# Kernel optimization log

Measured on AMD Instinct MI355X. Metric: run time of the kernel, lower is better.

## Reference

```python
import jax, jax.numpy as jnp
import numpy as np

EPS = 1e-12  # matches torch F.normalize default eps
TARGET_N = 6.0  # target_compression_N


def _l2_normalize(v):
    n = jnp.linalg.norm(v, axis=-1, keepdims=True)
    return v / jnp.maximum(n, EPS)


def setup_inputs() -> dict:
    key = jax.random.key(0)
    k1, k2, k3 = jax.random.split(key, 3)
    B, L, D = 4, 8192, 1024
    x = jax.random.normal(k1, (B, L, D), dtype=jnp.float32)
    # nn.Linear weights (out, in), applied as x @ W.T
    Wq = jax.random.normal(k2, (D, D), dtype=jnp.float32) * (1.0 / np.sqrt(D))
    Wk = jax.random.normal(k3, (D, D), dtype=jnp.float32) * (1.0 / np.sqrt(D))
    return {"x": x, "Wq": Wq, "Wk": Wk}


def reference(x, Wq, Wk):
    B, L, D = x.shape
    q = jnp.einsum('bld,ed->ble', x, Wq)
    k = jnp.einsum('bld,ed->ble', x, Wk)
    q_norm = _l2_normalize(q)
    k_norm = _l2_normalize(k)
    k_prev = jnp.roll(k_norm, shift=1, axis=1)
    cos_sim = jnp.sum(q_norm * k_prev, axis=-1)          # (B, L)
    p = 0.5 * (1.0 - cos_sim)
    p = p.at[:, 0].set(1.0)
    b = (p >= 0.5).astype(x.dtype)
    b = b.at[:, 0].set(1.0)

    F_val = jnp.mean(b)
    G_val = jnp.mean(p)
    N = TARGET_N
    ratio_loss = N / (N - 1.0) * ((N - 1.0) * F_val * G_val + (1.0 - F_val) * (1.0 - G_val))

    # Stream compaction via cumsum-based scatter.  Lc_max is data dependent in
    # the torch code; for jit-compatibility we pad the compressed axis to L.
    mask = b > 0.5                                        # (B, L) bool
    dest = jnp.cumsum(b.astype(jnp.int32), axis=1) - 1   # destination slot per boundary
    dest = jnp.clip(dest, 0, L - 1)
    bidx = jnp.broadcast_to(jnp.arange(B, dtype=jnp.int32)[:, None], (B, L))
    # Non-boundary positions contribute exact zeros (x * mask), so colliding
    # destinations from clipped/non-boundary entries are harmless under add.
    x_down = jnp.zeros((B, L, D), dtype=x.dtype).at[bidx, dest].add(x * mask[..., None])
    P_down = jnp.zeros((B, L), dtype=p.dtype).at[bidx, dest].add(p * mask)
    lengths = jnp.sum(b, axis=1).astype(jnp.int32)        # (B,)

    return x_down, P_down, b, p, lengths, ratio_loss
```

## Files before the change

### kernel.cpp

```cpp
#include <hip/hip_runtime.h>
#include <stdint.h>
#include <stddef.h>

typedef __attribute__((ext_vector_type(8)))  _Float16 f16x8;
typedef __attribute__((ext_vector_type(16))) float    f32x16;
typedef __attribute__((ext_vector_type(4)))  float    f32x4;
typedef __attribute__((ext_vector_type(4)))  unsigned int u32x4;

#define B_ 4
#define L_ 8192
#define D_ 1024
#define BL 32768
#define XR 32768
#define XCV_BYTES (256u * XR * 16u)
#define WCV_BYTES (256u * 1024u * 16u)

__device__ __forceinline__ void gload16(const void* g, void* l){
  __builtin_amdgcn_global_load_lds((const __attribute__((address_space(1))) void*)g,
                                   (__attribute__((address_space(3))) void*)l, 16, 0, 0);
}

__device__ __forceinline__ f32x16 MF(f16x8 a, f16x8 b, f32x16 c){
  return __builtin_amdgcn_mfma_f32_32x32x16_f16(a, b, c, 0, 0, 0);
}

__global__ void k0_cvt(const float* __restrict__ x, const float* __restrict__ Wq,
                       const float* __restrict__ Wk, unsigned char* __restrict__ xcv)
{
  __shared__ unsigned short hi[64][128];
  __shared__ unsigned short lo[64][128];
  const int bx = blockIdx.x, kt = blockIdx.y, tid = threadIdx.x;
  const float* src; unsigned char* dst; int rs, rt;
  if (bx < 512){ src = x;  dst = xcv;                         rs = XR;   rt = bx; }
  else if (bx < 528){ src = Wq; dst = xcv + XCV_BYTES;        rs = 1024; rt = bx - 512; }
  else { src = Wk; dst = xcv + XCV_BYTES + WCV_BYTES;         rs = 1024; rt = bx - 528; }

  #pragma unroll
  for (int it = 0; it < 8; ++it){
    int idx = it*256 + tid;
    int r = idx >> 5, q4 = idx & 31;
    f32x4 v = *(const f32x4*)(src + (size_t)(rt*64 + r)*1024 + kt*128 + q4*4);
    int swb = ((q4 >> 1) ^ (r & 15))*8 + (q4 & 1)*4;
    #pragma unroll
    for (int j = 0; j < 4; ++j){
      float f = v[j];
      _Float16 h = (_Float16)f;
      _Float16 l = (_Float16)(f - (float)h);
      hi[r][swb + j] = __builtin_bit_cast(unsigned short, h);
      lo[r][swb + j] = __builtin_bit_cast(unsigned short, l);
    }
  }
  __syncthreads();
  #pragma unroll
  for (int it = 0; it < 8; ++it){
    int seg = it*4 + (tid >> 6);
    int r = tid & 63;
    int ksl = seg >> 3, c = seg & 7;
    const unsigned short* plane = (c < 4) ? &hi[0][0] : &lo[0][0];
    int kl = ksl*32 + (c & 3)*8;
    u32x4 val = *(const u32x4*)(plane + r*128 + ((((kl >> 3) ^ (r & 15))) << 3));
    int P = (kt*4 + ksl)*8 + c;
    *(u32x4*)(dst + ((size_t)P * rs + rt*64 + r) * 16) = val;
  }
}

__launch_bounds__(512, 2)
__global__ void k1_f16(const unsigned char* __restrict__ xcv,
                       float* __restrict__ dotP, float* __restrict__ nqP,
                       float* __restrict__ nkP,
                       float* __restrict__ qface, float* __restrict__ kface)
{
  __shared__ __align__(16) unsigned char lds[131072];
  const int tid = threadIdx.x, lane = tid & 63, w = tid >> 6;
  const int wr = w >> 1, wc = w & 1, l31 = lane & 31, lh = lane >> 5;
  const int bid = blockIdx.x;
  const int strip = (bid & 7) + ((bid >> 6) << 3);
  const int ec = (bid >> 3) & 7;
  const int row0 = strip << 8, col0 = ec << 7;

  unsigned goff[4]; int loff[4]; unsigned d0[4], d1[4];
  #pragma unroll
  for (int j = 0; j < 4; ++j){
    int cj = w*4 + j;
    if (cj < 16){
      int lp = cj >> 2, sub = cj & 3;
      int cg = (lp & 1) + ((lp >> 1) << 2);
      goff[j] = ((unsigned)cg * XR + (unsigned)(row0 + sub*64 + lane)) * 16u;
      loff[j] = lp*4096 + (sub*64 + lane)*16;
      d0[j] = 2u*XR*16u; d1[j] = 6u*XR*16u;
    } else if (cj < 24){
      int t = cj - 16, lp = t >> 1, hf = t & 1;
      int cg = (lp & 1) + ((lp >> 1) << 2);
      goff[j] = XCV_BYTES + ((unsigned)cg * 1024u + (unsigned)(col0 + hf*64 + lane)) * 16u;
      loff[j] = 16384 + lp*2048 + (hf*64 + lane)*16;
      d0[j] = 32768u; d1[j] = 98304u;
    } else {
      int t = cj - 24, lp = t >> 1, hf = t & 1;
      int cg = (lp & 1) + ((lp >> 1) << 2);
      goff[j] = XCV_BYTES + WCV_BYTES + ((unsigned)cg * 1024u + (unsigned)(col0 + hf*64 + lane)) * 16u;
      loff[j] = 24576 + lp*2048 + (hf*64 + lane)*16;
      d0[j] = 32768u; d1[j] = 98304u;
    }
  }

  #define STAGE(slot) { _Pragma("unroll") \
    for (int j = 0; j < 4; ++j) gload16(xcv + goff[j], lds + (slot) + loff[j]); }
  #define ADV(par) { _Pragma("unroll") \
    for (int j = 0; j < 4; ++j) goff[j] += (par) ? d1[j] : d0[j]; }

  STAGE(0u)      ADV(0)
  STAGE(32768u)  ADV(1)
  STAGE(65536u)  ADV(0)

  const unsigned ab = (unsigned)(lh*4096) + (unsigned)((wr*64 + l31)*16);
  const unsigned bb = 16384u + (unsigned)(lh*2048) + (unsigned)((wc*64 + l31)*16);

  f32x16 accq[2][2] = {}, acck[2][2] = {};

  for (int h = 0; h < 64; ++h){
    if (h < 62)      { asm volatile("s_waitcnt vmcnt(8)" ::: "memory"); }
    else if (h == 62){ asm volatile("s_waitcnt vmcnt(4)" ::: "memory"); }
    else             { asm volatile("s_waitcnt vmcnt(0)" ::: "memory"); }
    __builtin_amdgcn_s_barrier();
    if (h < 61){ unsigned s3 = (unsigned)((h+3) & 3) * 32768u; STAGE(s3) ADV((h+3) & 1) }
    const unsigned cur = (unsigned)(h & 3) * 32768u;
    f16x8 ah[2], al[2];
    ah[0] = *(const f16x8*)(lds + cur + ab);
    ah[1] = *(const f16x8*)(lds + cur + ab + 512u);
    al[0] = *(const f16x8*)(lds + cur + ab + 8192u);
    al[1] = *(const f16x8*)(lds + cur + ab + 8704u);
    #pragma unroll
    for (int n = 0; n < 2; ++n){
      unsigned bo = cur + bb + (unsigned)n*512u;
      f16x8 qh = *(const f16x8*)(lds + bo);
      f16x8 ql = *(const f16x8*)(lds + bo + 4096u);
      f16x8 kh = *(const f16x8*)(lds + bo + 8192u);
      f16x8 kl_ = *(const f16x8*)(lds + bo + 12288u);
      __builtin_amdgcn_s_setprio(1);
      #pragma unroll
      for (int mt = 0; mt < 2; ++mt){
        accq[mt][n] = MF(ah[mt], qh, accq[mt][n]);
        accq[mt][n] = MF(ah[mt], ql, accq[mt][n]);
        accq[mt][n] = MF(al[mt], qh, accq[mt][n]);
        acck[mt][n] = MF(ah[mt], kh, acck[mt][n]);
        acck[mt][n] = MF(ah[mt], kl_, acck[mt][n]);
        acck[mt][n] = MF(al[mt], kh, acck[mt][n]);
      }
      __builtin_amdgcn_s_setprio(0);
    }
  }

  __syncthreads();
  float* kbuf = (float*)lds;
  #pragma unroll
  for (int mt = 0; mt < 2; ++mt)
    #pragma unroll
    for (int r = 0; r < 16; ++r){
      int rm = (r & 3) + ((r >> 2) << 3) + (lh << 2);
      int rl = wr*64 + mt*32 + rm;
      kbuf[rl*128 + wc*64 + l31]      = acck[mt][0][r];
      kbuf[rl*128 + wc*64 + 32 + l31] = acck[mt][1][r];
    }
  __syncthreads();
  f32x16 dvv[2], qvv[2], kvv[2];
  #pragma unroll
  for (int mt = 0; mt < 2; ++mt){
    qvv[mt] = accq[mt][0]*accq[mt][0] + accq[mt][1]*accq[mt][1];
    kvv[mt] = acck[mt][0]*acck[mt][0] + acck[mt][1]*acck[mt][1];
    #pragma unroll
    for (int r = 0; r < 16; ++r){
      int rm = (r & 3) + ((r >> 2) << 3) + (lh << 2);
      int rl = wr*64 + mt*32 + rm;
      int cl = rl - 1; if (cl < 0) cl = 0;
      float k0v = kbuf[cl*128 + wc*64 + l31];
      float k1v = kbuf[cl*128 + wc*64 + 32 + l31];
      dvv[mt][r] = accq[mt][0][r]*k0v + accq[mt][1][r]*k1v;
    }
  }
  __syncthreads();
  if (wr == 0 && lh == 0){
    qface[strip*1024 + ec*128 + wc*64 + l31]      = accq[0][0][0];
    qface[strip*1024 + ec*128 + wc*64 + 32 + l31] = accq[0][1][0];
  }
  if (wr == 3 && lh == 1){
    kface[strip*1024 + ec*128 + wc*64 + l31]      = acck[1][0][15];
    kface[strip*1024 + ec*128 + wc*64 + 32 + l31] = acck[1][1][15];
  }
  #pragma unroll
  for (int m = 1; m < 32; m <<= 1){
    #pragma unroll
    for (int mt = 0; mt < 2; ++mt)
      #pragma unroll
      for (int r = 0; r < 16; ++r){
        dvv[mt][r] += __shfl_xor(dvv[mt][r], m, 64);
        qvv[mt][r] += __shfl_xor(qvv[mt][r], m, 64);
        kvv[mt][r] += __shfl_xor(kvv[mt][r], m, 64);
      }
  }
  float* scr = (float*)lds;
  if (l31 == 0 && wc == 1){
    #pragma unroll
    for (int mt = 0; mt < 2; ++mt)
      #pragma unroll
      for (int r = 0; r < 16; ++r){
        int rm = (r & 3) + ((r >> 2) << 3) + (lh << 2);
        int ti = (wr*2 + mt)*32 + rm;
        scr[ti] = dvv[mt][r]; scr[256 + ti] = qvv[mt][r]; scr[512 + ti] = kvv[mt][r];
      }
  }
  __syncthreads();
  if (l31 == 0 && wc == 0){
    #pragma unroll
    for (int mt = 0; mt < 2; ++mt)
      #pragma unroll
      for (int r = 0; r < 16; ++r){
        int rm = (r & 3) + ((r >> 2) << 3) + (lh << 2);
        int ti = (wr*2 + mt)*32 + rm;
        size_t idx = (size_t)ec * BL + row0 + wr*64 + mt*32 + rm;
        dotP[idx] = dvv[mt][r] + scr[ti];
        nqP[idx]  = qvv[mt][r] + scr[256 + ti];
        nkP[idx]  = kvv[mt][r] + scr[512 + ti];
      }
  }
}

__global__ void k15_reduce(float* __restrict__ dotP, float* __restrict__ nqP,
                           float* __restrict__ nkP)
{
  int idx = blockIdx.x*1024 + threadIdx.x;
  float* base = (idx < 32768) ? dotP : (idx < 65536 ? nqP : nkP);
  int row = idx & 32767;
  float s = 0.f;
  #pragma unroll
  for (int e = 0; e < 8; ++e) s += base[(size_t)e*BL + row];
  base[row] = s;
}

__global__ void k2_scan(const float* __restrict__ dotF, const float* __restrict__ nqF,
                        const float* __restrict__ nkF,
                        const float* __restrict__ qface, const float* __restrict__ kface,
                        float* __restrict__ p_out, float* __restrict__ b_out,
                        float* __restrict__ len_out, int* __restrict__ invmap,
                        float* __restrict__ bat_sums, int* __restrict__ lenI)
{
  const int batch = blockIdx.x;
  const int tid   = threadIdx.x;
  const int lane  = tid & 63, wv = tid >> 6;
  const int lb    = tid << 3;
  const int g0    = batch * L_ + lb;

  float dta[8], nqa[8], nka[8];
  *(f32x4*)(dta)   = *(const f32x4*)(dotF + g0); *(f32x4*)(dta+4) = *(const f32x4*)(dotF + g0 + 4);
  *(f32x4*)(nqa)   = *(const f32x4*)(nqF + g0);  *(f32x4*)(nqa+4) = *(const f32x4*)(nqF + g0 + 4);
  *(f32x4*)(nka)   = *(const f32x4*)(nkF + g0);  *(f32x4*)(nka+4) = *(const f32x4*)(nkF + g0 + 4);
  float nkp = (lb > 0) ? nkF[g0 - 1] : 0.f;

  float ps = 0.f; int bc = 0; unsigned bits = 0;
  #pragma unroll
  for (int j = 0; j < 8; ++j){
    const int l = lb + j;
    const int g = batch * L_ + l;
    float p;
    if (l == 0) p = 1.f;
    else {
      float dt = dta[j];
      if ((l & 255) == 0){
        int s = g >> 8;
        const f32x4* qf = (const f32x4*)(qface + (size_t)s*1024);
        const f32x4* kf = (const f32x4*)(kface + (size_t)(s-1)*1024);
        f32x4 a4 = {0.f,0.f,0.f,0.f};
        for (int i = 0; i < 256; ++i) a4 += qf[i]*kf[i];
        dt = a4[0] + a4[1] + a4[2] + a4[3];
      }
      float nkprev = j ? nka[j-1] : nkp;
      float dn = fmaxf(sqrtf(nqa[j]), 1e-12f) * fmaxf(sqrtf(nkprev), 1e-12f);
      p = 0.5f * (1.f - dt/dn);
    }
    const int bb = (p >= 0.5f) ? 1 : 0;
    p_out[g] = p;
    b_out[g] = (float)bb;
    ps += p; bc += bb; bits |= (unsigned)bb << j;
  }
  int sc = bc;
  #pragma unroll
  for (int m = 1; m < 64; m <<= 1){
    int t = __shfl_up(sc, m, 64);
    if (lane >= m) sc += t;
  }
  float pss = ps;
  #pragma unroll
  for (int m = 1; m < 64; m <<= 1) pss += __shfl_xor(pss, m, 64);

  __shared__ int wsum[16];
  __shared__ float wps[16];
  if (lane == 63) wsum[wv] = sc;
  if (lane == 0)  wps[wv] = pss;
  __syncthreads();
  if (tid < 16){
    int v = wsum[tid];
    #pragma unroll
    for (int m = 1; m < 16; m <<= 1){
      int t = __shfl_up(v, m, 64);
      if (tid >= m) v += t;
    }
    wsum[tid] = v;
  }
  __syncthreads();
  const int waveoff = (wv == 0) ? 0 : wsum[wv - 1];
  const int total = wsum[15];
  int run = waveoff + sc - bc;
  #pragma unroll
  for (int j = 0; j < 8; ++j){
    if ((bits >> j) & 1u){ invmap[batch * L_ + run] = lb + j; ++run; }
  }
  if (tid == 0){
    float psum = 0.f;
    #pragma unroll
    for (int i = 0; i < 16; ++i) psum += wps[i];
    bat_sums[batch]     = (float)total;
    bat_sums[4 + batch] = psum;
    lenI[batch]    = total;
    len_out[batch] = (float)total;
  }
}

__global__ void k3_fill(const float* __restrict__ x, const float* __restrict__ p_out,
                        const int* __restrict__ invmap, const int* __restrict__ lenI,
                        const float* __restrict__ bat_sums,
                        float* __restrict__ xdown, float* __restrict__ Pdown,
                        float* __restrict__ loss_out)
{
  const int bid = blockIdx.x, tid = threadIdx.x;
  #pragma unroll 4
  for (int i = 0; i < 16; ++i){
    const int s = bid*16 + i;
    const int batch = s >> 13, j = s & 8191;
    const int len = lenI[batch];
    const int inb = (j < len) ? 1 : 0;
    const int src = inb ? invmap[batch * L_ + j] : 0;
    f32x4 v = {0.f, 0.f, 0.f, 0.f};
    if (inb) v = *(const f32x4*)(x + (((size_t)(batch * L_ + src)) << 10) + (tid << 2));
    *(f32x4*)(xdown + (((size_t)(batch * L_ + j)) << 10) + (tid << 2)) = v;
    if (tid == 0) Pdown[batch * L_ + j] = inb ? p_out[batch * L_ + src] : 0.f;
  }
  if (bid == 0 && tid == 0){
    const float F = (bat_sums[0] + bat_sums[1] + bat_sums[2] + bat_sums[3]) * (1.f / 32768.f);
    const float G = (bat_sums[4] + bat_sums[5] + bat_sums[6] + bat_sums[7]) * (1.f / 32768.f);
    loss_out[0] = 1.2f * (5.f * F * G + (1.f - F) * (1.f - G));
  }
}

extern "C" void kernel_launch(void* const* d_in, const int* in_sizes, int n_in,
                              void* d_out, int out_size, void* d_ws, size_t ws_size,
                              hipStream_t stream)
{
  const float* x  = (const float*)d_in[0];
  const float* Wq = (const float*)d_in[1];
  const float* Wk = (const float*)d_in[2];

  float* out      = (float*)d_out;
  float* xdown    = out;
  float* Pdown    = out + (size_t)BL * D_;
  float* b_out    = Pdown + BL;
  float* p_out    = b_out + BL;
  float* len_out  = p_out + BL;
  float* loss_out = len_out + B_;

  float* qface = xdown + (size_t)4*1024*1024;
  float* kface = qface + 131072;

  unsigned char* xcv = (unsigned char*)d_ws;
  float* dotP     = (float*)(xcv + XCV_BYTES + 2*WCV_BYTES);
  float* nqP      = dotP + (size_t)8*BL;
  float* nkP      = nqP + (size_t)8*BL;
  int*   invmap   = (int*)(nkP + (size_t)8*BL);
  float* bat_sums = (float*)(invmap + BL);
  int*   lenI     = (int*)(bat_sums + 8);

  hipLaunchKernelGGL(k0_cvt, dim3(544, 8), dim3(256), 0, stream, x, Wq, Wk, xcv);
  hipLaunchKernelGGL(k1_f16, dim3(1024), dim3(512), 0, stream,
                     xcv, dotP, nqP, nkP, qface, kface);
  hipLaunchKernelGGL(k15_reduce, dim3(96), dim3(1024), 0, stream, dotP, nqP, nkP);
  hipLaunchKernelGGL(k2_scan, dim3(4), dim3(1024), 0, stream,
                     dotP, nqP, nkP, qface, kface,
                     p_out, b_out, len_out, invmap, bat_sums, lenI);
  hipLaunchKernelGGL(k3_fill, dim3(2048), dim3(256), 0, stream,
                     x, p_out, invmap, lenI, bat_sums, xdown, Pdown, loss_out);
}
```

Baseline: 716.1 us.

## Split Q/K columns across wave columns and parallelize strip-boundary face dots

In the fused GEMM kernel, each wave column now computes four 32-column tiles of either Q or K rather than two tiles of both. This changes the B-operand LDS addressing and the epilogue: K waves stage their tile to LDS, Q waves compute the shifted dot products, and one cross-wave scratch exchange and barrier are removed. The serial 256-iteration strip-boundary q·k dot products are also moved out of the single-block-per-batch scan kernel into extra blocks of the reduce kernel, one wave per strip. This adds a small facedot buffer in the workspace.

New measurement: 666.3 us. -7.0%, faster.

```diff
diff --git a/kernel.cpp b/kernel.cpp
--- a/kernel.cpp
+++ b/kernel.cpp
@@ -112,10 +112,10 @@
   STAGE(32768u)  ADV(1)
   STAGE(65536u)  ADV(0)
 
-  const unsigned ab = (unsigned)(lh*4096) + (unsigned)((wr*64 + l31)*16);
-  const unsigned bb = 16384u + (unsigned)(lh*2048) + (unsigned)((wc*64 + l31)*16);
-
-  f32x16 accq[2][2] = {}, acck[2][2] = {};
+  const unsigned ab  = (unsigned)(lh*4096) + (unsigned)((wr*64 + l31)*16);
+  const unsigned bb0 = 16384u + (unsigned)(wc*8192) + (unsigned)(lh*2048) + (unsigned)(l31*16);
+
+  f32x16 acc[2][4] = {};
 
   for (int h = 0; h < 64; ++h){
     if (h < 62)      { asm volatile("s_waitcnt vmcnt(8)" ::: "memory"); }
@@ -130,21 +130,16 @@
     al[0] = *(const f16x8*)(lds + cur + ab + 8192u);
     al[1] = *(const f16x8*)(lds + cur + ab + 8704u);
     #pragma unroll
-    for (int n = 0; n < 2; ++n){
-      unsigned bo = cur + bb + (unsigned)n*512u;
-      f16x8 qh = *(const f16x8*)(lds + bo);
-      f16x8 ql = *(const f16x8*)(lds + bo + 4096u);
-      f16x8 kh = *(const f16x8*)(lds + bo + 8192u);
-      f16x8 kl_ = *(const f16x8*)(lds + bo + 12288u);
+    for (int n = 0; n < 4; ++n){
+      unsigned bo = cur + bb0 + (unsigned)n*512u;
+      f16x8 bh = *(const f16x8*)(lds + bo);
+      f16x8 bl = *(const f16x8*)(lds + bo + 4096u);
       __builtin_amdgcn_s_setprio(1);
       #pragma unroll
       for (int mt = 0; mt < 2; ++mt){
-        accq[mt][n] = MF(ah[mt], qh, accq[mt][n]);
-        accq[mt][n] = MF(ah[mt], ql, accq[mt][n]);
-        accq[mt][n] = MF(al[mt], qh, accq[mt][n]);
-        acck[mt][n] = MF(ah[mt], kh, acck[mt][n]);
-        acck[mt][n] = MF(ah[mt], kl_, acck[mt][n]);
-        acck[mt][n] = MF(al[mt], kh, acck[mt][n]);
+        acc[mt][n] = MF(ah[mt], bh, acc[mt][n]);
+        acc[mt][n] = MF(ah[mt], bl, acc[mt][n]);
+        acc[mt][n] = MF(al[mt], bh, acc[mt][n]);
       }
       __builtin_amdgcn_s_setprio(0);
     }
@@ -152,93 +147,108 @@
 
   __syncthreads();
   float* kbuf = (float*)lds;
-  #pragma unroll
-  for (int mt = 0; mt < 2; ++mt)
-    #pragma unroll
-    for (int r = 0; r < 16; ++r){
-      int rm = (r & 3) + ((r >> 2) << 3) + (lh << 2);
-      int rl = wr*64 + mt*32 + rm;
-      kbuf[rl*128 + wc*64 + l31]      = acck[mt][0][r];
-      kbuf[rl*128 + wc*64 + 32 + l31] = acck[mt][1][r];
-    }
-  __syncthreads();
-  f32x16 dvv[2], qvv[2], kvv[2];
+  if (wc == 1){
+    #pragma unroll
+    for (int mt = 0; mt < 2; ++mt)
+      #pragma unroll
+      for (int n = 0; n < 4; ++n)
+        #pragma unroll
+        for (int r = 0; r < 16; ++r){
+          int rm = (r & 3) + ((r >> 2) << 3) + (lh << 2);
+          int rl = wr*64 + mt*32 + rm;
+          kbuf[rl*128 + n*32 + l31] = acc[mt][n][r];
+        }
+  }
+  __syncthreads();
+
+  if (wc == 0 && wr == 0 && lh == 0){
+    #pragma unroll
+    for (int n = 0; n < 4; ++n)
+      qface[strip*1024 + ec*128 + n*32 + l31] = acc[0][n][0];
+  }
+  if (wc == 1 && wr == 3 && lh == 1){
+    #pragma unroll
+    for (int n = 0; n < 4; ++n)
+      kface[strip*1024 + ec*128 + n*32 + l31] = acc[1][n][15];
+  }
+
+  f32x16 dv[2], sv[2];
   #pragma unroll
   for (int mt = 0; mt < 2; ++mt){
-    qvv[mt] = accq[mt][0]*accq[mt][0] + accq[mt][1]*accq[mt][1];
-    kvv[mt] = acck[mt][0]*acck[mt][0] + acck[mt][1]*acck[mt][1];
-    #pragma unroll
-    for (int r = 0; r < 16; ++r){
-      int rm = (r & 3) + ((r >> 2) << 3) + (lh << 2);
-      int rl = wr*64 + mt*32 + rm;
-      int cl = rl - 1; if (cl < 0) cl = 0;
-      float k0v = kbuf[cl*128 + wc*64 + l31];
-      float k1v = kbuf[cl*128 + wc*64 + 32 + l31];
-      dvv[mt][r] = accq[mt][0][r]*k0v + accq[mt][1][r]*k1v;
-    }
-  }
-  __syncthreads();
-  if (wr == 0 && lh == 0){
-    qface[strip*1024 + ec*128 + wc*64 + l31]      = accq[0][0][0];
-    qface[strip*1024 + ec*128 + wc*64 + 32 + l31] = accq[0][1][0];
-  }
-  if (wr == 3 && lh == 1){
-    kface[strip*1024 + ec*128 + wc*64 + l31]      = acck[1][0][15];
-    kface[strip*1024 + ec*128 + wc*64 + 32 + l31] = acck[1][1][15];
-  }
-  #pragma unroll
-  for (int m = 1; m < 32; m <<= 1){
-    #pragma unroll
-    for (int mt = 0; mt < 2; ++mt)
-      #pragma unroll
-      for (int r = 0; r < 16; ++r){
-        dvv[mt][r] += __shfl_xor(dvv[mt][r], m, 64);
-        qvv[mt][r] += __shfl_xor(qvv[mt][r], m, 64);
-        kvv[mt][r] += __shfl_xor(kvv[mt][r], m, 64);
-      }
-  }
-  float* scr = (float*)lds;
-  if (l31 == 0 && wc == 1){
-    #pragma unroll
-    for (int mt = 0; mt < 2; ++mt)
+    sv[mt] = acc[mt][0]*acc[mt][0] + acc[mt][1]*acc[mt][1]
+           + acc[mt][2]*acc[mt][2] + acc[mt][3]*acc[mt][3];
+    if (wc == 0){
       #pragma unroll
       for (int r = 0; r < 16; ++r){
         int rm = (r & 3) + ((r >> 2) << 3) + (lh << 2);
-        int ti = (wr*2 + mt)*32 + rm;
-        scr[ti] = dvv[mt][r]; scr[256 + ti] = qvv[mt][r]; scr[512 + ti] = kvv[mt][r];
+        int rl = wr*64 + mt*32 + rm;
+        int cl = rl - 1; if (cl < 0) cl = 0;
+        float s = 0.f;
+        #pragma unroll
+        for (int n = 0; n < 4; ++n)
+          s += acc[mt][n][r] * kbuf[cl*128 + n*32 + l31];
+        dv[mt][r] = s;
       }
-  }
-  __syncthreads();
-  if (l31 == 0 && wc == 0){
+    }
+  }
+  #pragma unroll
+  for (int m = 1; m < 32; m <<= 1){
+    #pragma unroll
+    for (int mt = 0; mt < 2; ++mt)
+      #pragma unroll
+      for (int r = 0; r < 16; ++r){
+        sv[mt][r] += __shfl_xor(sv[mt][r], m, 64);
+        if (wc == 0) dv[mt][r] += __shfl_xor(dv[mt][r], m, 64);
+      }
+  }
+  if (l31 == 0){
     #pragma unroll
     for (int mt = 0; mt < 2; ++mt)
       #pragma unroll
       for (int r = 0; r < 16; ++r){
         int rm = (r & 3) + ((r >> 2) << 3) + (lh << 2);
-        int ti = (wr*2 + mt)*32 + rm;
         size_t idx = (size_t)ec * BL + row0 + wr*64 + mt*32 + rm;
-        dotP[idx] = dvv[mt][r] + scr[ti];
-        nqP[idx]  = qvv[mt][r] + scr[256 + ti];
-        nkP[idx]  = kvv[mt][r] + scr[512 + ti];
+        if (wc == 0){ dotP[idx] = dv[mt][r]; nqP[idx] = sv[mt][r]; }
+        else        { nkP[idx] = sv[mt][r]; }
       }
   }
 }
 
 __global__ void k15_reduce(float* __restrict__ dotP, float* __restrict__ nqP,
-                           float* __restrict__ nkP)
-{
-  int idx = blockIdx.x*1024 + threadIdx.x;
-  float* base = (idx < 32768) ? dotP : (idx < 65536 ? nqP : nkP);
-  int row = idx & 32767;
-  float s = 0.f;
-  #pragma unroll
-  for (int e = 0; e < 8; ++e) s += base[(size_t)e*BL + row];
-  base[row] = s;
+                           float* __restrict__ nkP,
+                           const float* __restrict__ qface,
+                           const float* __restrict__ kface,
+                           float* __restrict__ facedot)
+{
+  const int b = blockIdx.x, tid = threadIdx.x;
+  if (b < 96){
+    int idx = b*1024 + tid;
+    float* base = (idx < 32768) ? dotP : (idx < 65536 ? nqP : nkP);
+    int row = idx & 32767;
+    float s = 0.f;
+    #pragma unroll
+    for (int e = 0; e < 8; ++e) s += base[(size_t)e*BL + row];
+    base[row] = s;
+  } else {
+    const int lane = tid & 63, wv = tid >> 6;
+    const int s = (b - 96)*16 + wv;
+    float acc4 = 0.f;
+    if (s > 0){
+      const f32x4* qf = (const f32x4*)(qface + (size_t)s*1024);
+      const f32x4* kf = (const f32x4*)(kface + (size_t)(s-1)*1024);
+      f32x4 a = {0.f,0.f,0.f,0.f};
+      #pragma unroll
+      for (int i = 0; i < 4; ++i) a += qf[lane*4 + i] * kf[lane*4 + i];
+      acc4 = a[0] + a[1] + a[2] + a[3];
+    }
+    #pragma unroll
+    for (int m = 1; m < 64; m <<= 1) acc4 += __shfl_xor(acc4, m, 64);
+    if (lane == 0) facedot[s] = acc4;
+  }
 }
 
 __global__ void k2_scan(const float* __restrict__ dotF, const float* __restrict__ nqF,
-                        const float* __restrict__ nkF,
-                        const float* __restrict__ qface, const float* __restrict__ kface,
+                        const float* __restrict__ nkF, const float* __restrict__ facedot,
                         float* __restrict__ p_out, float* __restrict__ b_out,
                         float* __restrict__ len_out, int* __restrict__ invmap,
                         float* __restrict__ bat_sums, int* __restrict__ lenI)
@@ -263,15 +273,7 @@
     float p;
     if (l == 0) p = 1.f;
     else {
-      float dt = dta[j];
-      if ((l & 255) == 0){
-        int s = g >> 8;
-        const f32x4* qf = (const f32x4*)(qface + (size_t)s*1024);
-        const f32x4* kf = (const f32x4*)(kface + (size_t)(s-1)*1024);
-        f32x4 a4 = {0.f,0.f,0.f,0.f};
-        for (int i = 0; i < 256; ++i) a4 += qf[i]*kf[i];
-        dt = a4[0] + a4[1] + a4[2] + a4[3];
-      }
+      float dt = ((l & 255) == 0) ? facedot[g >> 8] : dta[j];
       float nkprev = j ? nka[j-1] : nkp;
       float dn = fmaxf(sqrtf(nqa[j]), 1e-12f) * fmaxf(sqrtf(nkprev), 1e-12f);
       p = 0.5f * (1.f - dt/dn);
@@ -376,13 +378,15 @@
   int*   invmap   = (int*)(nkP + (size_t)8*BL);
   float* bat_sums = (float*)(invmap + BL);
   int*   lenI     = (int*)(bat_sums + 8);
+  float* facedot  = (float*)(lenI + 4);
 
   hipLaunchKernelGGL(k0_cvt, dim3(544, 8), dim3(256), 0, stream, x, Wq, Wk, xcv);
   hipLaunchKernelGGL(k1_f16, dim3(1024), dim3(512), 0, stream,
                      xcv, dotP, nqP, nkP, qface, kface);
-  hipLaunchKernelGGL(k15_reduce, dim3(96), dim3(1024), 0, stream, dotP, nqP, nkP);
+  hipLaunchKernelGGL(k15_reduce, dim3(104), dim3(1024), 0, stream,
+                     dotP, nqP, nkP, qface, kface, facedot);
   hipLaunchKernelGGL(k2_scan, dim3(4), dim3(1024), 0, stream,
-                     dotP, nqP, nkP, qface, kface,
+                     dotP, nqP, nkP, facedot,
                      p_out, b_out, len_out, invmap, bat_sums, lenI);
   hipLaunchKernelGGL(k3_fill, dim3(2048), dim3(256), 0, stream,
                      x, p_out, invmap, lenI, bat_sums, xdown, Pdown, loss_out);
```
